# Kernel optimization log

Hardware: AMD Instinct MI355X
Metric: run time of the kernel (lower is better)

The kernel has to match this reference:

```python
import jax, jax.numpy as jnp
import numpy as np

N_NODES = 50000
N_EDGES = 800000
F_DIM = 64


def setup_inputs() -> dict:
    key = jax.random.key(0)
    ks = jax.random.split(key, 11)
    inp = {
        "x": jax.random.normal(ks[0], (1,), dtype=jnp.float32),  # unused by the module
        "features": jax.random.normal(ks[1], (N_NODES, F_DIM), dtype=jnp.float32),
        "edge_index": jax.random.randint(ks[2], (2, N_EDGES), 0, N_NODES, dtype=jnp.int64),
        # Conv2d(1, 8, (2,1)) -> weight (8,1,2,1) flattened to (8,2)
        "conv_w": jax.random.normal(ks[3], (8, 2), dtype=jnp.float32) * (1.0 / np.sqrt(2.0)),
        "conv_b": jax.random.normal(ks[4], (8,), dtype=jnp.float32) * 0.1,
        "w1": jax.random.normal(ks[5], (16, F_DIM), dtype=jnp.float32) * (1.0 / np.sqrt(F_DIM)),
        "b1": jax.random.normal(ks[6], (16,), dtype=jnp.float32) * 0.1,
        "w2": jax.random.normal(ks[7], (1, 16), dtype=jnp.float32) * (1.0 / np.sqrt(16.0)),
        "b2": jax.random.normal(ks[8], (1,), dtype=jnp.float32) * 0.1,
        "w3": jax.random.normal(ks[9], (1, 8), dtype=jnp.float32) * (1.0 / np.sqrt(8.0)),
        "b3": jax.random.normal(ks[10], (1,), dtype=jnp.float32) * 0.1,
    }
    return inp


def reference(x, features, edge_index, conv_w, conv_b, w1, b1, w2, b2, w3, b3):
    # Gather endpoint features for each edge: (E, F) each
    src, dst = edge_index[0], edge_index[1]
    f1 = features[src]
    f2 = features[dst]
    # Conv2d(1,8,(2,1)) on (E,1,2,F) collapses the 2-row stack:
    # out[e,o,f] = w[o,0]*f1[e,f] + w[o,1]*f2[e,f] + b[o]
    feat = (f1[:, None, :] * conv_w[None, :, 0, None]
            + f2[:, None, :] * conv_w[None, :, 1, None]
            + conv_b[None, :, None])          # (E, 8, F)
    feat = jax.nn.relu(feat)
    # fc1: Linear(F, 16) applied over last dim -> (E, 8, 16)
    feat = jax.nn.relu(jnp.einsum('eof,gf->eog', feat, w1) + b1)
    # fc2: Linear(16, 1) -> (E, 8, 1) -> reshape (E, 8)
    feat = jax.nn.relu(jnp.einsum('eog,hg->eoh', feat, w2) + b2)
    feat = feat.reshape(-1, 8)
    # fc3: Linear(8, 1) + sigmoid -> (E, 1)
    out = jax.nn.sigmoid(feat @ w3.T + b3)
    return out
```

## Files before the change

kernel.cpp:

```cpp
#include <hip/hip_runtime.h>
#include <hip/hip_bf16.h>


typedef _Float16 f16x8 __attribute__((ext_vector_type(8)));
typedef _Float16 f16x4 __attribute__((ext_vector_type(4)));
typedef _Float16 f16x2 __attribute__((ext_vector_type(2)));
typedef short    bf16x8 __attribute__((ext_vector_type(8)));
typedef float    f32x4  __attribute__((ext_vector_type(4)));
typedef float    f32x2  __attribute__((ext_vector_type(2)));

union U8 { f16x8 v; f16x2 p[4]; };

static __device__ __forceinline__ short f2bf(float f) {
    union { __hip_bfloat16 h; short s; } u;
    u.h = __float2bfloat16(f);
    return u.s;
}

__global__ __launch_bounds__(256) void feat_to_f16(const float* __restrict__ in,
                                                   _Float16* __restrict__ out,
                                                   int n4) {
    int i = blockIdx.x * blockDim.x + threadIdx.x;
    const int stride = gridDim.x * blockDim.x;
    for (; i < n4; i += stride) {
        const f32x4 v = ((const f32x4*)in)[i];
        ((f16x4*)out)[i] = __builtin_convertvector(v, f16x4);
    }
}

__global__ __launch_bounds__(256, 4) void edgeconv_f16_g8(
    const _Float16* __restrict__ feat16,
    const int*      __restrict__ edge_index,
    const float* __restrict__ conv_w, const float* __restrict__ conv_b,
    const float* __restrict__ w1,     const float* __restrict__ b1,
    const float* __restrict__ w2,     const float* __restrict__ b2,
    const float* __restrict__ w3,     const float* __restrict__ b3,
    float* __restrict__ out, int nEdges)
{
    __shared__ __align__(16) char smem[4][2][2][1024];

    const int tid = threadIdx.x;
    const int l   = tid & 63;
    const int wid = tid >> 6;
    const int grp = l >> 4;
    const int n   = l & 15;
    const int ch  = l & 7;
    const int el  = (l >> 3) & 1;
    const int chunk = l & 7;
    const int rr    = l >> 3;
    const int eloc  = rr >> 1;
    const int endp  = rr & 1;

    const float* w1r = w1 + n * 64 + grp * 8;
    f16x8 aw0, aw1;
    #pragma unroll
    for (int i = 0; i < 8; ++i) {
        aw0[i] = (_Float16)w1r[i];
        aw1[i] = (_Float16)w1r[32 + i];
    }

    const _Float16 cah = (_Float16)conv_w[2 * ch];
    const _Float16 cch = (_Float16)conv_w[2 * ch + 1];
    const _Float16 cbh = (_Float16)conv_b[ch];
    const f16x2 vca = {cah, cah}, vcc = {cch, cch}, vcb = {cbh, cbh};
    const f16x2 vzero = {(_Float16)0.f, (_Float16)0.f};

    f32x4 accInit;
    float w2r[4];
    #pragma unroll
    for (int r = 0; r < 4; ++r) {
        accInit[r] = b1[grp * 4 + r];
        w2r[r]     = w2[grp * 4 + r];
    }
    const float w3v = w3[ch];
    const float b2v = b2[0];
    const float b3v = b3[0];

    const int nGroups    = (nEdges + 7) >> 3;
    const int totalWaves = gridDim.x * 4;
    int g = blockIdx.x * 4 + wid;
    if (g >= nGroups) return;

    char* base0 = (char*)&smem[wid][0][0][0];
    char* base1 = (char*)&smem[wid][1][0][0];

#define ISSUE(VS, VD, BUF) do { \
    _Pragma("unroll") \
    for (int p_ = 0; p_ < 2; ++p_) { \
        const int si_  = __shfl((VS), 4 * p_ + eloc); \
        const int di_  = __shfl((VD), 4 * p_ + eloc); \
        const int idx_ = endp ? di_ : si_; \
        const char* ga_ = (const char*)feat16 \
                        + (size_t)(unsigned)idx_ * 128u + chunk * 16; \
        __builtin_amdgcn_global_load_lds( \
            (const __attribute__((address_space(1))) void*)ga_, \
            (__attribute__((address_space(3))) void*)((BUF) + p_ * 1024), \
            16, 0, 0); \
    } \
} while (0)

    int ce = min(g * 8 + (l & 7), nEdges - 1);
    int vs = edge_index[ce];
    int vd = edge_index[nEdges + ce];
    ISSUE(vs, vd, base0);

    int gn = g + totalWaves;
    int vs1 = 0, vd1 = 0;
    if (gn < nGroups) {
        const int cen = min(gn * 8 + (l & 7), nEdges - 1);
        vs1 = edge_index[cen];
        vd1 = edge_index[nEdges + cen];
    }

    int cur = 0;
    while (true) {
        const bool more = (gn < nGroups);

        if (more) {
            ISSUE(vs1, vd1, (cur ? base0 : base1));
            __builtin_amdgcn_sched_barrier(0);
            asm volatile("s_waitcnt vmcnt(2)" ::: "memory");
        } else {
            asm volatile("s_waitcnt vmcnt(0)" ::: "memory");
        }
        __builtin_amdgcn_sched_barrier(0);

        const int g2 = gn + totalWaves;
        int vs2 = 0, vd2 = 0;
        if (g2 < nGroups) {
            const int ce2 = min(g2 * 8 + (l & 7), nEdges - 1);
            vs2 = edge_index[ce2];
            vd2 = edge_index[nEdges + ce2];
        }

        const char* myBuf = cur ? base1 : base0;
        float zp[4];
        #pragma unroll
        for (int t = 0; t < 4; ++t) {
            const int p = t >> 1;
            const int q = t & 1;
            const char* pb = myBuf + p * 1024;
            const int roff = q * 512 + el * 256 + grp * 16;
            U8 s0_, s1_, d0_, d1_, c0, c1;
            s0_.v = *(const f16x8*)(pb + roff);
            s1_.v = *(const f16x8*)(pb + roff + 64);
            d0_.v = *(const f16x8*)(pb + roff + 128);
            d1_.v = *(const f16x8*)(pb + roff + 192);

            #pragma unroll
            for (int pp = 0; pp < 4; ++pp) {
                f16x2 tL = __builtin_elementwise_fma(vca, s0_.p[pp],
                            __builtin_elementwise_fma(vcc, d0_.p[pp], vcb));
                c0.p[pp] = __builtin_elementwise_max(tL, vzero);
                f16x2 tH = __builtin_elementwise_fma(vca, s1_.p[pp],
                            __builtin_elementwise_fma(vcc, d1_.p[pp], vcb));
                c1.p[pp] = __builtin_elementwise_max(tH, vzero);
            }

            f32x4 acc = accInit;
            acc = __builtin_amdgcn_mfma_f32_16x16x32_f16(aw0, c0.v, acc, 0, 0, 0);
            acc = __builtin_amdgcn_mfma_f32_16x16x32_f16(aw1, c1.v, acc, 0, 0, 0);

            float z_ = 0.f;
            #pragma unroll
            for (int r = 0; r < 4; ++r) {
                const float h1 = fmaxf(acc[r], 0.f);
                z_ = fmaf(h1, w2r[r], z_);
            }
            zp[t] = z_;
        }

        #pragma unroll
        for (int t = 0; t < 4; ++t) zp[t] += __shfl_xor(zp[t], 16);
        #pragma unroll
        for (int t = 0; t < 4; ++t) zp[t] += __shfl_xor(zp[t], 32);
        #pragma unroll
        for (int t = 0; t < 4; ++t) {
            const float h2 = fmaxf(zp[t] + b2v, 0.f);
            zp[t] = h2 * w3v;
        }
        #pragma unroll
        for (int t = 0; t < 4; ++t) zp[t] += __shfl_xor(zp[t], 1);
        #pragma unroll
        for (int t = 0; t < 4; ++t) zp[t] += __shfl_xor(zp[t], 2);
        #pragma unroll
        for (int t = 0; t < 4; ++t) zp[t] += __shfl_xor(zp[t], 4);
        #pragma unroll
        for (int t = 0; t < 4; ++t) {
            const float z  = zp[t] + b3v;
            const float sg = 1.0f / (1.0f + __expf(-z));
            if ((l & 55) == 0) {
                const int e = g * 8 + 2 * t + (l >> 3);
                if (e < nEdges) out[e] = sg;
            }
        }

        if (!more) break;
        g = gn; gn = g2; vs1 = vs2; vd1 = vd2; cur ^= 1;
    }
#undef ISSUE
}

__global__ __launch_bounds__(256) void edgeconv_mfma2(
    const float* __restrict__ features, const int* __restrict__ edge_index,
    const float* __restrict__ conv_w, const float* __restrict__ conv_b,
    const float* __restrict__ w1, const float* __restrict__ b1,
    const float* __restrict__ w2, const float* __restrict__ b2,
    const float* __restrict__ w3, const float* __restrict__ b3,
    float* __restrict__ out, int nEdges)
{
    const int tid = threadIdx.x;
    const int l   = tid & 63;
    const int wid = tid >> 6;
    const int grp = l >> 4;
    const int n   = l & 15;
    const int ch  = l & 7;
    const int el  = (l >> 3) & 1;

    const float* w1r = w1 + n * 64 + grp * 8;
    bf16x8 aw0, aw1;
    #pragma unroll
    for (int i = 0; i < 8; ++i) {
        aw0[i] = f2bf(w1r[i]);
        aw1[i] = f2bf(w1r[32 + i]);
    }
    const float ca = conv_w[2 * ch];
    const float cc = conv_w[2 * ch + 1];
    const float cb = conv_b[ch];
    float b1r[4], w2r[4];
    #pragma unroll
    for (int r = 0; r < 4; ++r) { b1r[r] = b1[grp * 4 + r]; w2r[r] = w2[grp * 4 + r]; }
    const float w3v = w3[ch];
    const float b2v = b2[0];
    const float b3v = b3[0];

    const int ebase = (blockIdx.x * 4 + wid) * 16;
    const int ce    = min(ebase + n, nEdges - 1);
    const int vs    = edge_index[ce];
    const int vd    = edge_index[nEdges + ce];

#define LOAD_TILE4(T, X1, X2) do { \
    const int sn_ = __shfl(vs, 2 * (T) + el); \
    const int dn_ = __shfl(vd, 2 * (T) + el); \
    const float* p1_ = features + (size_t)sn_ * 64 + grp * 8; \
    const float* p2_ = features + (size_t)dn_ * 64 + grp * 8; \
    X1[0] = *(const f32x4*)(p1_);      X1[1] = *(const f32x4*)(p1_ + 4); \
    X1[2] = *(const f32x4*)(p1_ + 32); X1[3] = *(const f32x4*)(p1_ + 36); \
    X2[0] = *(const f32x4*)(p2_);      X2[1] = *(const f32x4*)(p2_ + 4); \
    X2[2] = *(const f32x4*)(p2_ + 32); X2[3] = *(const f32x4*)(p2_ + 36); \
} while (0)

    f32x4 x1v[4], x2v[4];
    LOAD_TILE4(0, x1v, x2v);
    const f32x2 vca = {ca, ca}, vcc = {cc, cc}, vcb = {cb, cb};
    const f32x2 vz  = {0.f, 0.f};

    #pragma unroll
    for (int t = 0; t < 8; ++t) {
        f32x4 n1v[4], n2v[4];
        if (t < 7) LOAD_TILE4(t + 1, n1v, n2v);
        bf16x8 cf0, cf1;
        #pragma unroll
        for (int p = 0; p < 8; ++p) {
            const int q = p >> 1;
            const int o = (p & 1) * 2;
            f32x2 u = {x1v[q][o], x1v[q][o + 1]};
            f32x2 v = {x2v[q][o], x2v[q][o + 1]};
            f32x2 tt = __builtin_elementwise_fma(vca, u,
                        __builtin_elementwise_fma(vcc, v, vcb));
            tt = __builtin_elementwise_max(tt, vz);
            const short s0 = f2bf(tt[0]), s1 = f2bf(tt[1]);
            if (p < 4) { cf0[2 * (p & 3)] = s0; cf0[2 * (p & 3) + 1] = s1; }
            else       { cf1[2 * (p & 3)] = s0; cf1[2 * (p & 3) + 1] = s1; }
        }
        f32x4 acc = {0.f, 0.f, 0.f, 0.f};
        acc = __builtin_amdgcn_mfma_f32_16x16x32_bf16(aw0, cf0, acc, 0, 0, 0);
        acc = __builtin_amdgcn_mfma_f32_16x16x32_bf16(aw1, cf1, acc, 0, 0, 0);
        float zp = 0.f;
        #pragma unroll
        for (int r = 0; r < 4; ++r) {
            const float h1 = fmaxf(acc[r] + b1r[r], 0.f);
            zp = fmaf(h1, w2r[r], zp);
        }
        zp += __shfl_xor(zp, 16);
        zp += __shfl_xor(zp, 32);
        const float h2 = fmaxf(zp + b2v, 0.f);
        float t3 = h2 * w3v;
        t3 += __shfl_xor(t3, 1);
        t3 += __shfl_xor(t3, 2);
        t3 += __shfl_xor(t3, 4);
        const float z  = t3 + b3v;
        const float sg = 1.0f / (1.0f + __expf(-z));
        if ((l & 55) == 0) {
            const int e = ebase + 2 * t + (l >> 3);
            if (e < nEdges) out[e] = sg;
        }
        if (t < 7) {
            #pragma unroll
            for (int i = 0; i < 4; ++i) { x1v[i] = n1v[i]; x2v[i] = n2v[i]; }
        }
    }
#undef LOAD_TILE4
}

extern "C" void kernel_launch(void* const* d_in, const int* in_sizes, int n_in,
                              void* d_out, int out_size, void* d_ws, size_t ws_size,
                              hipStream_t stream) {
    const float* features = (const float*)d_in[1];
    const int*   edge_idx = (const int*)d_in[2];
    const float* conv_w   = (const float*)d_in[3];
    const float* conv_b   = (const float*)d_in[4];
    const float* w1       = (const float*)d_in[5];
    const float* b1       = (const float*)d_in[6];
    const float* w2       = (const float*)d_in[7];
    const float* b2       = (const float*)d_in[8];
    const float* w3       = (const float*)d_in[9];
    const float* b3       = (const float*)d_in[10];
    float*       out      = (float*)d_out;

    const int nEdges = in_sizes[2] / 2;
    const int nFeat  = in_sizes[1];

    const size_t need = (size_t)nFeat * sizeof(_Float16);
    if (ws_size >= need) {
        _Float16* feat16 = (_Float16*)d_ws;
        feat_to_f16<<<2048, 256, 0, stream>>>(features, feat16, nFeat / 4);
        const int nGroups = (nEdges + 7) >> 3;
        const int blocks  = min(2048, (nGroups + 3) / 4);
        edgeconv_f16_g8<<<blocks, 256, 0, stream>>>(feat16, edge_idx,
                                                    conv_w, conv_b, w1, b1, w2, b2, w3, b3,
                                                    out, nEdges);
    } else {
        const dim3 grid((nEdges + 63) / 64);
        edgeconv_mfma2<<<grid, 256, 0, stream>>>(features, edge_idx,
                                                 conv_w, conv_b, w1, b1, w2, b2, w3, b3,
                                                 out, nEdges);
    }
}
```

Baseline: 79.69 us.

## Switch edge MLP to 32x32x16 MFMA with swizzled LDS layout

Replaces the pair of 16x16x32 MFMAs per half-tile with four 32x32x16 MFMAs per 4-edge tile, where N covers 4 edges times 8 conv channels and M is the 16 fc1 outputs padded to 32. Gathered feature chunks are stored in LDS with a rotated (swizzled) chunk order so that the per-lane reads avoid bank conflicts. Bias add moves after the MFMA, and the shuffle reduction is shortened to match the new lane mapping. The grid is capped at 1024 blocks instead of 2048. Half of the M dimension is zero padding, so MFMA work is wasted, and the fp32 accumulator per lane grows to 16 registers.

```diff
diff --git a/kernel.cpp b/kernel.cpp
--- a/kernel.cpp
+++ b/kernel.cpp
@@ -8,6 +8,7 @@
 typedef short    bf16x8 __attribute__((ext_vector_type(8)));
 typedef float    f32x4  __attribute__((ext_vector_type(4)));
 typedef float    f32x2  __attribute__((ext_vector_type(2)));
+typedef float    f32x16 __attribute__((ext_vector_type(16)));
 
 union U8 { f16x8 v; f16x2 p[4]; };
 
@@ -28,7 +29,7 @@
     }
 }
 
-__global__ __launch_bounds__(256, 4) void edgeconv_f16_g8(
+__global__ __launch_bounds__(256, 4) void edgeconv_f16_m32(
     const _Float16* __restrict__ feat16,
     const int*      __restrict__ edge_index,
     const float* __restrict__ conv_w, const float* __restrict__ conv_b,
@@ -42,21 +43,27 @@
     const int tid = threadIdx.x;
     const int l   = tid & 63;
     const int wid = tid >> 6;
-    const int grp = l >> 4;
-    const int n   = l & 15;
-    const int ch  = l & 7;
-    const int el  = (l >> 3) & 1;
-    const int chunk = l & 7;
-    const int rr    = l >> 3;
-    const int eloc  = rr >> 1;
-    const int endp  = rr & 1;
-
-    const float* w1r = w1 + n * 64 + grp * 8;
-    f16x8 aw0, aw1;
-    #pragma unroll
-    for (int i = 0; i < 8; ++i) {
-        aw0[i] = (_Float16)w1r[i];
-        aw1[i] = (_Float16)w1r[32 + i];
+    const int n   = l & 31;
+    const int h   = l >> 5;
+    const int ch  = n & 7;
+    const int et  = n >> 3;
+    const int chunk  = l & 7;
+    const int rr     = l >> 3;
+    const int eloc   = rr >> 1;
+    const int endp   = rr & 1;
+    const int gchunk = (chunk + rr) & 7;
+
+    f16x8 aw[4];
+    #pragma unroll
+    for (int j = 0; j < 4; ++j)
+        #pragma unroll
+        for (int i = 0; i < 8; ++i) aw[j][i] = (_Float16)0.f;
+    if (n < 16) {
+        const float* w1r = w1 + n * 64 + h * 8;
+        #pragma unroll
+        for (int j = 0; j < 4; ++j)
+            #pragma unroll
+            for (int i = 0; i < 8; ++i) aw[j][i] = (_Float16)w1r[j * 16 + i];
     }
 
     const _Float16 cah = (_Float16)conv_w[2 * ch];
@@ -65,16 +72,22 @@
     const f16x2 vca = {cah, cah}, vcc = {cch, cch}, vcb = {cbh, cbh};
     const f16x2 vzero = {(_Float16)0.f, (_Float16)0.f};
 
-    f32x4 accInit;
-    float w2r[4];
+    float b1r[8], w2r[8];
     #pragma unroll
     for (int r = 0; r < 4; ++r) {
-        accInit[r] = b1[grp * 4 + r];
-        w2r[r]     = w2[grp * 4 + r];
+        b1r[r]     = b1[4 * h + r];      w2r[r]     = w2[4 * h + r];
+        b1r[4 + r] = b1[8 + 4 * h + r];  w2r[4 + r] = w2[8 + 4 * h + r];
     }
     const float w3v = w3[ch];
     const float b2v = b2[0];
     const float b3v = b3[0];
+
+    int soff[4], doff[4];
+    #pragma unroll
+    for (int j = 0; j < 4; ++j) {
+        soff[j] = et * 256       + (((2 * j + h - 2 * et)     & 7) << 4);
+        doff[j] = et * 256 + 128 + (((2 * j + h - 2 * et - 1) & 7) << 4);
+    }
 
     const int nGroups    = (nEdges + 7) >> 3;
     const int totalWaves = gridDim.x * 4;
@@ -91,7 +104,7 @@
         const int di_  = __shfl((VD), 4 * p_ + eloc); \
         const int idx_ = endp ? di_ : si_; \
         const char* ga_ = (const char*)feat16 \
-                        + (size_t)(unsigned)idx_ * 128u + chunk * 16; \
+                        + (size_t)(unsigned)idx_ * 128u + gchunk * 16; \
         __builtin_amdgcn_global_load_lds( \
             (const __attribute__((address_space(1))) void*)ga_, \
             (__attribute__((address_space(3))) void*)((BUF) + p_ * 1024), \
@@ -134,63 +147,52 @@
         }
 
         const char* myBuf = cur ? base1 : base0;
-        float zp[4];
-        #pragma unroll
-        for (int t = 0; t < 4; ++t) {
-            const int p = t >> 1;
-            const int q = t & 1;
-            const char* pb = myBuf + p * 1024;
-            const int roff = q * 512 + el * 256 + grp * 16;
-            U8 s0_, s1_, d0_, d1_, c0, c1;
-            s0_.v = *(const f16x8*)(pb + roff);
-            s1_.v = *(const f16x8*)(pb + roff + 64);
-            d0_.v = *(const f16x8*)(pb + roff + 128);
-            d1_.v = *(const f16x8*)(pb + roff + 192);
-
+        float zp[2];
+        #pragma unroll
+        for (int t = 0; t < 2; ++t) {
+            const char* pb = myBuf + t * 1024;
+            f32x16 acc = {};
             #pragma unroll
-            for (int pp = 0; pp < 4; ++pp) {
-                f16x2 tL = __builtin_elementwise_fma(vca, s0_.p[pp],
-                            __builtin_elementwise_fma(vcc, d0_.p[pp], vcb));
-                c0.p[pp] = __builtin_elementwise_max(tL, vzero);
-                f16x2 tH = __builtin_elementwise_fma(vca, s1_.p[pp],
-                            __builtin_elementwise_fma(vcc, d1_.p[pp], vcb));
-                c1.p[pp] = __builtin_elementwise_max(tH, vzero);
+            for (int j = 0; j < 4; ++j) {
+                U8 s_, d_, c_;
+                s_.v = *(const f16x8*)(pb + soff[j]);
+                d_.v = *(const f16x8*)(pb + doff[j]);
+                #pragma unroll
+                for (int pp = 0; pp < 4; ++pp) {
+                    f16x2 tt = __builtin_elementwise_fma(vca, s_.p[pp],
+                                __builtin_elementwise_fma(vcc, d_.p[pp], vcb));
+                    c_.p[pp] = __builtin_elementwise_max(tt, vzero);
+                }
+                acc = __builtin_amdgcn_mfma_f32_32x32x16_f16(aw[j], c_.v, acc, 0, 0, 0);
             }
-
-            f32x4 acc = accInit;
-            acc = __builtin_amdgcn_mfma_f32_16x16x32_f16(aw0, c0.v, acc, 0, 0, 0);
-            acc = __builtin_amdgcn_mfma_f32_16x16x32_f16(aw1, c1.v, acc, 0, 0, 0);
-
             float z_ = 0.f;
             #pragma unroll
-            for (int r = 0; r < 4; ++r) {
-                const float h1 = fmaxf(acc[r], 0.f);
+            for (int r = 0; r < 8; ++r) {
+                const float h1 = fmaxf(acc[r] + b1r[r], 0.f);
                 z_ = fmaf(h1, w2r[r], z_);
             }
             zp[t] = z_;
         }
 
         #pragma unroll
-        for (int t = 0; t < 4; ++t) zp[t] += __shfl_xor(zp[t], 16);
-        #pragma unroll
-        for (int t = 0; t < 4; ++t) zp[t] += __shfl_xor(zp[t], 32);
-        #pragma unroll
-        for (int t = 0; t < 4; ++t) {
+        for (int t = 0; t < 2; ++t) zp[t] += __shfl_xor(zp[t], 32);
+        #pragma unroll
+        for (int t = 0; t < 2; ++t) {
             const float h2 = fmaxf(zp[t] + b2v, 0.f);
             zp[t] = h2 * w3v;
         }
         #pragma unroll
-        for (int t = 0; t < 4; ++t) zp[t] += __shfl_xor(zp[t], 1);
-        #pragma unroll
-        for (int t = 0; t < 4; ++t) zp[t] += __shfl_xor(zp[t], 2);
-        #pragma unroll
-        for (int t = 0; t < 4; ++t) zp[t] += __shfl_xor(zp[t], 4);
-        #pragma unroll
-        for (int t = 0; t < 4; ++t) {
+        for (int t = 0; t < 2; ++t) zp[t] += __shfl_xor(zp[t], 1);
+        #pragma unroll
+        for (int t = 0; t < 2; ++t) zp[t] += __shfl_xor(zp[t], 2);
+        #pragma unroll
+        for (int t = 0; t < 2; ++t) zp[t] += __shfl_xor(zp[t], 4);
+        #pragma unroll
+        for (int t = 0; t < 2; ++t) {
             const float z  = zp[t] + b3v;
             const float sg = 1.0f / (1.0f + __expf(-z));
-            if ((l & 55) == 0) {
-                const int e = g * 8 + 2 * t + (l >> 3);
+            if ((l & 39) == 0) {
+                const int e = g * 8 + t * 4 + et;
                 if (e < nEdges) out[e] = sg;
             }
         }
@@ -326,10 +328,10 @@
         _Float16* feat16 = (_Float16*)d_ws;
         feat_to_f16<<<2048, 256, 0, stream>>>(features, feat16, nFeat / 4);
         const int nGroups = (nEdges + 7) >> 3;
-        const int blocks  = min(2048, (nGroups + 3) / 4);
-        edgeconv_f16_g8<<<blocks, 256, 0, stream>>>(feat16, edge_idx,
-                                                    conv_w, conv_b, w1, b1, w2, b2, w3, b3,
-                                                    out, nEdges);
+        const int blocks  = min(1024, (nGroups + 3) / 4);
+        edgeconv_f16_m32<<<blocks, 256, 0, stream>>>(feat16, edge_idx,
+                                                     conv_w, conv_b, w1, b1, w2, b2, w3, b3,
+                                                     out, nEdges);
     } else {
         const dim3 grid((nEdges + 63) / 64);
         edgeconv_mfma2<<<grid, 256, 0, stream>>>(features, edge_idx,
```

Measured after the change: 72.34 us. 9.2% less time.
